# Kernel optimization log

Measured on AMD Instinct MI355X. Metric: run time of the kernel, lower is better.

Reference implementation:

```python
import jax, jax.numpy as jnp
import numpy as np
import math

ORIG_FREQ = 16000
NEW_FREQ = 14400
LPW = 6           # lowpass_filter_width


def _filter_params():
    """Replicates Resample._indices_and_weights with numpy (static constants)."""
    base = math.gcd(ORIG_FREQ, NEW_FREQ)
    conv_stride = ORIG_FREQ // base          # input samples per unit
    output_samples = NEW_FREQ // base        # polyphase count P
    min_freq = min(ORIG_FREQ, NEW_FREQ)
    lc = 0.99 * 0.5 * min_freq               # lowpass cutoff
    ww = LPW / (2.0 * lc)                    # window half-width (seconds)
    output_t = np.arange(output_samples, dtype=np.float64) / NEW_FREQ
    min_i = np.ceil((output_t - ww) * ORIG_FREQ)
    max_i = np.floor((output_t + ww) * ORIG_FREQ)
    W = int((max_i - min_i + 1).max())       # max filter width
    j = np.arange(W, dtype=np.float64)
    input_index = min_i[:, None] + j[None, :]
    delta_t = input_index / ORIG_FREQ - output_t[:, None]
    weights = np.zeros_like(delta_t)
    inside = np.abs(delta_t) < ww
    weights[inside] = 0.5 * (1 + np.cos(2 * math.pi * lc / LPW * delta_t[inside]))
    zero = delta_t == 0.0
    nz = ~zero
    weights[nz] *= np.sin(2 * math.pi * lc * delta_t[nz]) / (math.pi * delta_t[nz])
    weights[zero] *= 2 * lc
    weights /= ORIG_FREQ
    return min_i.astype(np.int64), weights.astype(np.float32), output_samples, conv_stride


def _output_samples(n):
    """Replicates Resample._output_samples (LinearResample::GetNumOutputSamples)."""
    tick = ORIG_FREQ * NEW_FREQ // math.gcd(ORIG_FREQ, NEW_FREQ)
    interval = n * (tick // ORIG_FREQ)
    tpo = tick // NEW_FREQ
    last = interval // tpo
    if last * tpo == interval:
        last -= 1
    return last + 1


def setup_inputs() -> dict:
    key = jax.random.key(0)
    _, w, _, _ = _filter_params()
    waveforms = jax.random.normal(key, (16, 480000), dtype=jnp.float32)
    return {"waveforms": waveforms, "weights": jnp.asarray(w)}


def _resample(waveforms, weights):
    fi, _, P, stride = _filter_params()
    B, N = waveforms.shape
    W = weights.shape[1]
    tot = _output_samples(N)
    M = (tot - 1) // P + 1                   # conv outputs per phase
    left_pad = max(0, -int(fi.min()))
    need = int(fi.max()) + stride * (M - 1) + W
    right_pad = max(0, need - N)
    wav = jnp.pad(waveforms, ((0, 0), (left_pad, right_pad)))
    # output sample n = i + P*m (phase i, unit m) reads input window starting
    # at first_indices[i] + stride*m  -> static gather index table [P, M, W]
    idx = (fi[:, None, None] + left_pad
           + stride * np.arange(M, dtype=np.int64)[None, :, None]
           + np.arange(W, dtype=np.int64)[None, None, :]).astype(np.int32)
    g = wav[:, idx]                          # [B, P, M, W]
    out = jnp.einsum('bpmw,pw->bpm', g, weights)
    out = jnp.transpose(out, (0, 2, 1)).reshape(B, M * P)  # interleave phases
    return out[:, :tot]


def reference(waveforms, weights):
    return _resample(waveforms, weights)
```

## Files before the change

kernel.cpp:

```cpp
#include <hip/hip_runtime.h>


#define RS_TPB 256

__global__ __launch_bounds__(RS_TPB) void resample_kernel(
    const float* __restrict__ wav, const float* __restrict__ wgt,
    float* __restrict__ out, int N, int K, int TOT) {
  __shared__ float s_out[RS_TPB * 18];

  const int b = blockIdx.y;
  const int k0 = blockIdx.x * RS_TPB;
  const int tid = threadIdx.x;
  const int k = k0 + tid;
  const float* __restrict__ wrow = wav + (size_t)b * N;

  if (k < K) {
    const int abase = 20 * k - 8;
    float win[36];
    if (abase >= 0 && abase + 36 <= N) {
#pragma unroll
      for (int r = 0; r < 9; ++r) {
        const float4 v = *reinterpret_cast<const float4*>(wrow + abase + (r << 2));
        win[4 * r + 0] = v.x;
        win[4 * r + 1] = v.y;
        win[4 * r + 2] = v.z;
        win[4 * r + 3] = v.w;
      }
    } else {
#pragma unroll
      for (int i = 0; i < 36; ++i) {
        const int gi = abase + i;
        win[i] = (gi >= 0 && gi < N) ? wrow[gi] : 0.0f;
      }
    }
    const int OFF[9] = {0, 1, 2, 3, 4, 5, 6, 8, 9};
#pragma unroll
    for (int j = 0; j < 18; ++j) {
      const int o = OFF[j % 9] + 2 + 10 * (j / 9);
      const float* wp = &wgt[14 * (j % 9)];
      float acc = 0.0f;
#pragma unroll
      for (int w = 0; w < 14; ++w) acc = fmaf(win[o + w], wp[w], acc);
      s_out[tid * 18 + j] = acc;
    }
  }
  __syncthreads();

  int nk = K - k0;
  if (nk > RS_TPB) nk = RS_TPB;
  const int n_out = nk * 18;
  const size_t obase = (size_t)b * TOT + (size_t)k0 * 18;
  float* __restrict__ orow = out + obase;
  const int n4 = n_out >> 2;
  for (int i4 = tid; i4 < n4; i4 += RS_TPB) {
    const float4 v = *reinterpret_cast<const float4*>(&s_out[i4 << 2]);
    *reinterpret_cast<float4*>(orow + (i4 << 2)) = v;
  }
  for (int i = (n4 << 2) + tid; i < n_out; i += RS_TPB) orow[i] = s_out[i];
}

extern "C" void kernel_launch(void* const* d_in, const int* in_sizes, int n_in,
                              void* d_out, int out_size, void* d_ws, size_t ws_size,
                              hipStream_t stream) {
  const float* wav = (const float*)d_in[0];
  const float* wgt = (const float*)d_in[1];
  float* out = (float*)d_out;

  const int N = 480000;
  const int B = in_sizes[0] / N;
  const int TOT = out_size / B;
  const int K = (TOT + 17) / 18;

  dim3 grid((K + RS_TPB - 1) / RS_TPB, B);
  resample_kernel<<<grid, RS_TPB, 0, stream>>>(wav, wgt, out, N, K, TOT);
}
```

Baseline: 16.19 us.

## Compute four polyphase units per thread and store directly without LDS staging

Each thread now produces 36 outputs (four 9-sample units) from a 56-sample register window instead of 18 outputs from 36 samples. This cuts the overlapping window reloads and halves the thread count. The shared-memory staging and the __syncthreads are removed, and each thread writes its outputs straight to global memory as float4 stores. In exchange, each thread now writes a 144-byte contiguous run, so a wavefront's stores are strided rather than coalesced. The larger window also raises register pressure and leaves fewer blocks in the grid.

```diff
diff --git a/kernel.cpp b/kernel.cpp
--- a/kernel.cpp
+++ b/kernel.cpp
@@ -2,61 +2,56 @@
 
 
 #define RS_TPB 256
+#define RS_G 4
+#define RS_OPT (RS_G * 9)
+#define RS_WIN 56
 
 __global__ __launch_bounds__(RS_TPB) void resample_kernel(
     const float* __restrict__ wav, const float* __restrict__ wgt,
     float* __restrict__ out, int N, int K, int TOT) {
-  __shared__ float s_out[RS_TPB * 18];
+  const int b = blockIdx.y;
+  const int k = blockIdx.x * RS_TPB + threadIdx.x;
+  if (k >= K) return;
 
-  const int b = blockIdx.y;
-  const int k0 = blockIdx.x * RS_TPB;
-  const int tid = threadIdx.x;
-  const int k = k0 + tid;
   const float* __restrict__ wrow = wav + (size_t)b * N;
+  const int abase = 40 * k - 8;
 
-  if (k < K) {
-    const int abase = 20 * k - 8;
-    float win[36];
-    if (abase >= 0 && abase + 36 <= N) {
+  float win[RS_WIN];
+  if (abase >= 0 && abase + RS_WIN <= N) {
 #pragma unroll
-      for (int r = 0; r < 9; ++r) {
-        const float4 v = *reinterpret_cast<const float4*>(wrow + abase + (r << 2));
-        win[4 * r + 0] = v.x;
-        win[4 * r + 1] = v.y;
-        win[4 * r + 2] = v.z;
-        win[4 * r + 3] = v.w;
-      }
-    } else {
+    for (int r = 0; r < RS_WIN / 4; ++r) {
+      const float4 v = *reinterpret_cast<const float4*>(wrow + abase + (r << 2));
+      win[4 * r + 0] = v.x;
+      win[4 * r + 1] = v.y;
+      win[4 * r + 2] = v.z;
+      win[4 * r + 3] = v.w;
+    }
+  } else {
 #pragma unroll
-      for (int i = 0; i < 36; ++i) {
-        const int gi = abase + i;
-        win[i] = (gi >= 0 && gi < N) ? wrow[gi] : 0.0f;
-      }
+    for (int i = 0; i < RS_WIN; ++i) {
+      const int gi = abase + i;
+      win[i] = (gi >= 0 && gi < N) ? wrow[gi] : 0.0f;
     }
-    const int OFF[9] = {0, 1, 2, 3, 4, 5, 6, 8, 9};
+  }
+
+  const int OFF[9] = {0, 1, 2, 3, 4, 5, 6, 8, 9};
+  float* __restrict__ orow = out + (size_t)b * TOT + (size_t)k * RS_OPT;
 #pragma unroll
-    for (int j = 0; j < 18; ++j) {
-      const int o = OFF[j % 9] + 2 + 10 * (j / 9);
+  for (int g = 0; g < RS_OPT / 4; ++g) {
+    float4 o;
+    float* po = &o.x;
+#pragma unroll
+    for (int q = 0; q < 4; ++q) {
+      const int j = 4 * g + q;
+      const int oidx = OFF[j % 9] + 2 + 10 * (j / 9);
       const float* wp = &wgt[14 * (j % 9)];
       float acc = 0.0f;
 #pragma unroll
-      for (int w = 0; w < 14; ++w) acc = fmaf(win[o + w], wp[w], acc);
-      s_out[tid * 18 + j] = acc;
+      for (int w = 0; w < 14; ++w) acc = fmaf(win[oidx + w], wp[w], acc);
+      po[q] = acc;
     }
+    *reinterpret_cast<float4*>(orow + (g << 2)) = o;
   }
-  __syncthreads();
-
-  int nk = K - k0;
-  if (nk > RS_TPB) nk = RS_TPB;
-  const int n_out = nk * 18;
-  const size_t obase = (size_t)b * TOT + (size_t)k0 * 18;
-  float* __restrict__ orow = out + obase;
-  const int n4 = n_out >> 2;
-  for (int i4 = tid; i4 < n4; i4 += RS_TPB) {
-    const float4 v = *reinterpret_cast<const float4*>(&s_out[i4 << 2]);
-    *reinterpret_cast<float4*>(orow + (i4 << 2)) = v;
-  }
-  for (int i = (n4 << 2) + tid; i < n_out; i += RS_TPB) orow[i] = s_out[i];
 }
 
 extern "C" void kernel_launch(void* const* d_in, const int* in_sizes, int n_in,
@@ -69,7 +64,7 @@
   const int N = 480000;
   const int B = in_sizes[0] / N;
   const int TOT = out_size / B;
-  const int K = (TOT + 17) / 18;
+  const int K = (TOT + RS_OPT - 1) / RS_OPT;
 
   dim3 grid((K + RS_TPB - 1) / RS_TPB, B);
   resample_kernel<<<grid, RS_TPB, 0, stream>>>(wav, wgt, out, N, K, TOT);
```

Result: slower. 25.17 us (+55.5%).
